# Kernel tuning notes

Hardware: AMD Instinct MI355X
Metric: run time of the kernel (lower is better)

Reference implementation:

```python
import jax, jax.numpy as jnp
import numpy as np

B, S, E, H = 4, 2048, 1024, 16
D = E // H  # head_dim = 64

def setup_inputs() -> dict:
    key = jax.random.key(0)
    k1, k2, k3 = jax.random.split(key, 3)
    x = jax.random.normal(k1, (B, S, E), dtype=jnp.float32)
    # nn.Linear(E, 3E, bias=False): y = x @ W^T; we store W already transposed as [E, 3E]
    w_qkv = jax.random.normal(k2, (E, 3 * E), dtype=jnp.float32) * (E ** -0.5)
    w_out = jax.random.normal(k3, (E, E), dtype=jnp.float32) * (E ** -0.5)
    b_out = jnp.zeros((E,), dtype=jnp.float32)
    return {"x": x, "w_qkv": w_qkv, "w_out": w_out, "b_out": b_out}

def reference(x, w_qkv, w_out, b_out):
    b, s, e = x.shape
    h, d = H, e // H
    # qkv projection then rearrange 'b s (qkv h d) -> qkv b h s d'
    qkv = (x @ w_qkv).reshape(b, s, 3, h, d).transpose(2, 0, 3, 1, 4)
    q, k, v = qkv[0], qkv[1], qkv[2]            # each [b, h, s, d]
    scale = jnp.asarray(d, x.dtype) ** -0.5
    att = jnp.einsum('bhxd,bhyd->bhxy', q, k) * scale   # [b, h, s, s]
    att = jax.nn.softmax(att, axis=-1)
    o = jnp.einsum('bhxy,bhyd->bhxd', att, v)           # [b, h, s, d]
    o = o.transpose(0, 2, 1, 3).reshape(b, s, e)        # 'b h s d -> b s (h d)'
    return o @ w_out + b_out
```

## Files before the change

kernel.cpp:

```cpp
#include <hip/hip_runtime.h>
#include <cstdint>
#include <cstddef>


typedef __attribute__((ext_vector_type(8))) short short8;
typedef __attribute__((ext_vector_type(4))) float float4_;
typedef unsigned int u32;
typedef unsigned short u16;

__device__ __forceinline__ u16 f2b(float f) {
  u32 u = __float_as_uint(f);
  u += 0x7FFFu + ((u >> 16) & 1u);
  return (u16)(u >> 16);
}

__device__ __forceinline__ float fexp2(float x) {
#if __has_builtin(__builtin_amdgcn_exp2f)
  return __builtin_amdgcn_exp2f(x);
#else
  return exp2f(x);
#endif
}

__device__ __forceinline__ u32 pk_trunc(float lo, float hi) {
#if __has_builtin(__builtin_amdgcn_perm)
  return __builtin_amdgcn_perm(__float_as_uint(hi), __float_as_uint(lo), 0x07060302);
#else
  return (__float_as_uint(hi) & 0xFFFF0000u) | (__float_as_uint(lo) >> 16);
#endif
}

#if __has_builtin(__builtin_amdgcn_fdot2_f32_bf16)
typedef __bf16 bf16x2 __attribute__((ext_vector_type(2)));
__device__ __forceinline__ float accum_pk(u32 pk, float acc) {
  bf16x2 p = __builtin_bit_cast(bf16x2, pk);
  bf16x2 one = __builtin_bit_cast(bf16x2, (u32)0x3F803F80u);
  return __builtin_amdgcn_fdot2_f32_bf16(p, one, acc, false);
}
#else
__device__ __forceinline__ float accum_pk(u32 pk, float acc) {
  return acc + __uint_as_float(pk << 16) + __uint_as_float(pk & 0xFFFF0000u);
}
#endif

__device__ __forceinline__ void async_cp16(const void* g, void* l) {
  __builtin_amdgcn_global_load_lds(
      (const __attribute__((address_space(1))) u32*)g,
      (__attribute__((address_space(3))) u32*)l, 16, 0, 0);
}


__device__ __forceinline__ void transpose_block(const float* __restrict__ in,
                                                u16* __restrict__ out,
                                                int R, int C, int bx, int by,
                                                float t[32][33]) {
  int tx = threadIdx.x & 31, ty = threadIdx.x >> 5;
  int r0 = by * 32, c0 = bx * 32;
#pragma unroll
  for (int k = 0; k < 4; k++)
    t[ty + 8 * k][tx] = in[(size_t)(r0 + ty + 8 * k) * C + c0 + tx];
  __syncthreads();
#pragma unroll
  for (int k = 0; k < 4; k++)
    out[(size_t)(c0 + ty + 8 * k) * R + r0 + tx] = f2b(t[tx][ty + 8 * k]);
}

__global__ void prepass_kernel(const float* __restrict__ x, u16* __restrict__ Xb,
                               const float* __restrict__ wqkv, u16* __restrict__ Wqt,
                               const float* __restrict__ wout, u16* __restrict__ Wot) {
  __shared__ float t[32][33];
  int gid = blockIdx.x;
  if (gid < 8192) {
    int i = gid * 256 + threadIdx.x;
    float4 v = ((const float4*)x)[i];
    uint2 p;
    p.x = (u32)f2b(v.x) | ((u32)f2b(v.y) << 16);
    p.y = (u32)f2b(v.z) | ((u32)f2b(v.w) << 16);
    ((uint2*)Xb)[i] = p;
  } else if (gid < 11264) {
    int j = gid - 8192;
    transpose_block(wqkv, Wqt, 1024, 3072, j % 96, j / 96, t);
  } else {
    int j = gid - 11264;
    transpose_block(wout, Wot, 1024, 1024, j % 32, j / 32, t);
  }
}

__global__ void transpose_v(const u16* __restrict__ V, u16* __restrict__ Vt) {
  __shared__ u16 t[64][80];
  int bh = blockIdx.y, s0 = blockIdx.x * 64;
  const u16* Vh = V + (size_t)bh * 2048 * 64;
  u16* Vth = Vt + (size_t)bh * 64 * 2048;
  int tr = threadIdx.x >> 3;
  int tc = (threadIdx.x & 7) * 8;
#pragma unroll
  for (int p = 0; p < 2; p++) {
    int r = p * 32 + tr;
    *(uint4*)&t[r][tc] = *(const uint4*)(Vh + (size_t)(s0 + r) * 64 + tc);
  }
  __syncthreads();
#pragma unroll
  for (int p = 0; p < 2; p++) {
    int d = p * 32 + tr;
    u16 tmp[8];
#pragma unroll
    for (int k = 0; k < 8; k++) tmp[k] = t[tc + k][d];
    *(uint4*)(Vth + (size_t)d * 2048 + s0 + tc) = *(uint4*)tmp;
  }
}


__global__ __launch_bounds__(512, 2) void gemm_qkv_kernel(
    const u16* __restrict__ A, const u16* __restrict__ Bt,
    u16* __restrict__ QKV) {
  const int K = 1024;
  const int NT = 16;
  __shared__ short8 lA[2][1024];
  __shared__ short8 lB[3][2048];
  int tid = threadIdx.x;
  int wid = tid >> 6, l = tid & 63, lr = l & 15, lq = l >> 4;
  int wm = wid >> 2, wn = wid & 3;
  int gid = blockIdx.x;
  int xcd = gid & 7, j = gid >> 3;
  int nt = j % 12, mt = xcd * 8 + j / 12;
  int m0 = mt * 128, n0 = nt * 256;

  float4_ acc[4][4] = {};

  const u16* srcA[2];
  const u16* srcB[4];
#pragma unroll
  for (int s = 0; s < 2; s++) {
    int fl = s * 8 + wid;
    srcA[s] = A + (size_t)(m0 + (fl >> 1) * 16 + lr) * K + (fl & 1) * 32 + lq * 8;
  }
#pragma unroll
  for (int s = 0; s < 4; s++) {
    int fl = s * 8 + wid;
    srcB[s] = Bt + (size_t)(n0 + (fl >> 1) * 16 + lr) * K + (fl & 1) * 32 + lq * 8;
  }

  auto stageA = [&](int buf, int k0) {
#pragma unroll
    for (int s = 0; s < 2; s++)
      async_cp16(srcA[s] + k0, &lA[buf][(s * 8 + wid) * 64 + l]);
  };
  auto stageB = [&](int bb, int k0) {
#pragma unroll
    for (int s = 0; s < 4; s++)
      async_cp16(srcB[s] + k0, &lB[bb][(s * 8 + wid) * 64 + l]);
  };

  stageA(0, 0);
  stageB(0, 0);
  stageB(1, 64);
  asm volatile("s_waitcnt vmcnt(4)" ::: "memory");
  __builtin_amdgcn_s_barrier();

  for (int u = 0; u < NT; ++u) {
    int buf = u & 1;
    int vb = u % 3;
    int kA = (u + 1 < NT ? u + 1 : NT - 1) * 64;
    int kB = (u + 2 < NT ? u + 2 : NT - 1) * 64;
    short8 af[4], bf[4];

#pragma unroll
    for (int mf = 0; mf < 4; mf++) af[mf] = lA[buf][((wm * 4 + mf) * 2 + 0) * 64 + l];
#pragma unroll
    for (int nf = 0; nf < 4; nf++) bf[nf] = lB[vb][((wn * 4 + nf) * 2 + 0) * 64 + l];
    stageA(buf ^ 1, kA);
    __builtin_amdgcn_s_barrier();
    __builtin_amdgcn_s_setprio(1);
#pragma unroll
    for (int mf = 0; mf < 4; mf++)
#pragma unroll
      for (int nf = 0; nf < 4; nf++)
        acc[mf][nf] = __builtin_amdgcn_mfma_f32_16x16x32_bf16(af[mf], bf[nf], acc[mf][nf], 0, 0, 0);
    __builtin_amdgcn_s_setprio(0);
    __builtin_amdgcn_s_barrier();

#pragma unroll
    for (int mf = 0; mf < 4; mf++) af[mf] = lA[buf][((wm * 4 + mf) * 2 + 1) * 64 + l];
#pragma unroll
    for (int nf = 0; nf < 4; nf++) bf[nf] = lB[vb][((wn * 4 + nf) * 2 + 1) * 64 + l];
    stageB((u + 2) % 3, kB);
    __builtin_amdgcn_s_barrier();
    __builtin_amdgcn_s_setprio(1);
#pragma unroll
    for (int mf = 0; mf < 4; mf++)
#pragma unroll
      for (int nf = 0; nf < 4; nf++)
        acc[mf][nf] = __builtin_amdgcn_mfma_f32_16x16x32_bf16(af[mf], bf[nf], acc[mf][nf], 0, 0, 0);
    __builtin_amdgcn_s_setprio(0);
    asm volatile("s_waitcnt vmcnt(4)" ::: "memory");
    __builtin_amdgcn_s_barrier();
  }
  asm volatile("s_waitcnt vmcnt(0)" ::: "memory");

  const float qsc = 0.18033688011112042f;
#pragma unroll
  for (int nf = 0; nf < 4; nf++) {
    int gn = n0 + wn * 64 + nf * 16 + lr;
    int sel = gn >> 10;
    int h = (gn >> 6) & 15;
    int d = gn & 63;
    float sc = (sel == 0) ? qsc : 1.0f;
    u16* dst = QKV + (size_t)sel * 8388608 + ((size_t)h * 2048) * 64 + d;
#pragma unroll
    for (int mf = 0; mf < 4; mf++) {
#pragma unroll
      for (int r = 0; r < 4; r++) {
        int gm = m0 + wm * 64 + mf * 16 + lq * 4 + r;
        int b = gm >> 11, s = gm & 2047;
        dst[((size_t)b * 16 * 2048 + s) * 64] = f2b(acc[mf][nf][r] * sc);
      }
    }
  }
}


__global__ __launch_bounds__(512, 2) void gemm_out_kernel(
    const u16* __restrict__ A, const u16* __restrict__ Bt,
    const float* __restrict__ bias, float* __restrict__ out) {
  const int K = 1024;
  const int NT = 16;
  __shared__ short8 lA[2][1024];
  __shared__ short8 lB[3][2048];
  int tid = threadIdx.x;
  int wid = tid >> 6, l = tid & 63, lr = l & 15, lq = l >> 4;
  int wm = wid >> 2, wn = wid & 3;
  int gid = blockIdx.x;
  int xcd = gid & 7, j = gid >> 3;
  int nt = j % 4, mt = xcd * 8 + j / 4;
  int m0 = mt * 128, n0 = nt * 256;

  float4_ acc[4][4] = {};

  const u16* srcA[2];
  const u16* srcB[4];
#pragma unroll
  for (int s = 0; s < 2; s++) {
    int fl = s * 8 + wid;
    srcA[s] = A + (size_t)(m0 + (fl >> 1) * 16 + lr) * K + (fl & 1) * 32 + lq * 8;
  }
#pragma unroll
  for (int s = 0; s < 4; s++) {
    int fl = s * 8 + wid;
    srcB[s] = Bt + (size_t)(n0 + (fl >> 1) * 16 + lr) * K + (fl & 1) * 32 + lq * 8;
  }

  auto stageA = [&](int buf, int k0) {
#pragma unroll
    for (int s = 0; s < 2; s++)
      async_cp16(srcA[s] + k0, &lA[buf][(s * 8 + wid) * 64 + l]);
  };
  auto stageB = [&](int bb, int k0) {
#pragma unroll
    for (int s = 0; s < 4; s++)
      async_cp16(srcB[s] + k0, &lB[bb][(s * 8 + wid) * 64 + l]);
  };

  stageA(0, 0);
  stageB(0, 0);
  stageB(1, 64);
  asm volatile("s_waitcnt vmcnt(4)" ::: "memory");
  __builtin_amdgcn_s_barrier();

  for (int u = 0; u < NT; ++u) {
    int buf = u & 1;
    int vb = u % 3;
    int kA = (u + 1 < NT ? u + 1 : NT - 1) * 64;
    int kB = (u + 2 < NT ? u + 2 : NT - 1) * 64;
    short8 af[4], bf[4];

#pragma unroll
    for (int mf = 0; mf < 4; mf++) af[mf] = lA[buf][((wm * 4 + mf) * 2 + 0) * 64 + l];
#pragma unroll
    for (int nf = 0; nf < 4; nf++) bf[nf] = lB[vb][((wn * 4 + nf) * 2 + 0) * 64 + l];
    stageA(buf ^ 1, kA);
    __builtin_amdgcn_s_barrier();
    __builtin_amdgcn_s_setprio(1);
#pragma unroll
    for (int mf = 0; mf < 4; mf++)
#pragma unroll
      for (int nf = 0; nf < 4; nf++)
        acc[mf][nf] = __builtin_amdgcn_mfma_f32_16x16x32_bf16(af[mf], bf[nf], acc[mf][nf], 0, 0, 0);
    __builtin_amdgcn_s_setprio(0);
    __builtin_amdgcn_s_barrier();

#pragma unroll
    for (int mf = 0; mf < 4; mf++) af[mf] = lA[buf][((wm * 4 + mf) * 2 + 1) * 64 + l];
#pragma unroll
    for (int nf = 0; nf < 4; nf++) bf[nf] = lB[vb][((wn * 4 + nf) * 2 + 1) * 64 + l];
    stageB((u + 2) % 3, kB);
    __builtin_amdgcn_s_barrier();
    __builtin_amdgcn_s_setprio(1);
#pragma unroll
    for (int mf = 0; mf < 4; mf++)
#pragma unroll
      for (int nf = 0; nf < 4; nf++)
        acc[mf][nf] = __builtin_amdgcn_mfma_f32_16x16x32_bf16(af[mf], bf[nf], acc[mf][nf], 0, 0, 0);
    __builtin_amdgcn_s_setprio(0);
    asm volatile("s_waitcnt vmcnt(4)" ::: "memory");
    __builtin_amdgcn_s_barrier();
  }
  asm volatile("s_waitcnt vmcnt(0)" ::: "memory");

#pragma unroll
  for (int nf = 0; nf < 4; nf++) {
    int gn = n0 + wn * 64 + nf * 16 + lr;
    float bv = bias[gn];
#pragma unroll
    for (int mf = 0; mf < 4; mf++)
#pragma unroll
      for (int r = 0; r < 4; r++) {
        int gm = m0 + wm * 64 + mf * 16 + lq * 4 + r;
        out[(size_t)gm * 1024 + gn] = acc[mf][nf][r] + bv;
      }
  }
}


__global__ __launch_bounds__(256) void attn_kernel(
    const u16* __restrict__ Qb, const u16* __restrict__ Kb,
    const u16* __restrict__ Vt, u16* __restrict__ Ob) {
  const int S = 2048, D = 64;
  __shared__ short8 lK[2][512];
  __shared__ short8 lV[2][512];
  __shared__ __align__(16) u32 pb[4][16][20];
  int tid = threadIdx.x;
  int w = tid >> 6, l = tid & 63, lr = l & 15, lq = l >> 4;
  int gid = blockIdx.x;
  int xcd = gid & 7, j = gid >> 3;
  int bh = xcd * 8 + (j >> 4);
  int qblk = j & 15;
  int q0 = qblk * 128 + w * 32;
  const u16* Qh = Qb + (size_t)bh * S * D;
  const u16* Kh = Kb + (size_t)bh * S * D;
  const u16* Vh = Vt + (size_t)bh * D * S;

  short8 qf[2][2];
#pragma unroll
  for (int qg = 0; qg < 2; qg++) {
    qf[qg][0] = *(const short8*)(Qh + (q0 + qg * 16 + lr) * D + lq * 8);
    qf[qg][1] = *(const short8*)(Qh + (q0 + qg * 16 + lr) * D + 32 + lq * 8);
  }

  float ls[2][4] = {};
  float4_ o[2][4] = {};

  const u16* kg = Kh + (size_t)(((w >> 1) << 5) + 2 * lr + (w & 1)) * D + lq * 8;
  const u16* vg = Vh + (size_t)(w * 16 + lr) * S + lq * 8;

  auto stage = [&](int buf, int kv0) {
    async_cp16(kg + (size_t)kv0 * D, &lK[buf][(w * 2 + 0) * 64 + l]);
    async_cp16(kg + (size_t)kv0 * D + 32, &lK[buf][(w * 2 + 1) * 64 + l]);
    async_cp16(vg + kv0, &lV[buf][(w * 2 + 0) * 64 + l]);
    async_cp16(vg + kv0 + 32, &lV[buf][(w * 2 + 1) * 64 + l]);
  };

  auto compute = [&](int buf) {
#pragma unroll
    for (int sub = 0; sub < 2; sub++) {
      short8 ke0 = lK[buf][((sub * 2 + 0) * 2 + 0) * 64 + l];
      short8 ke1 = lK[buf][((sub * 2 + 0) * 2 + 1) * 64 + l];
      short8 ko0 = lK[buf][((sub * 2 + 1) * 2 + 0) * 64 + l];
      short8 ko1 = lK[buf][((sub * 2 + 1) * 2 + 1) * 64 + l];
#pragma unroll
      for (int qg = 0; qg < 2; qg++) {
        float4_ z = {0.f, 0.f, 0.f, 0.f};
        float4_ s0 = __builtin_amdgcn_mfma_f32_16x16x32_bf16(qf[qg][0], ke0, z, 0, 0, 0);
        s0 = __builtin_amdgcn_mfma_f32_16x16x32_bf16(qf[qg][1], ke1, s0, 0, 0, 0);
        float4_ s1 = __builtin_amdgcn_mfma_f32_16x16x32_bf16(qf[qg][0], ko0, z, 0, 0, 0);
        s1 = __builtin_amdgcn_mfma_f32_16x16x32_bf16(qf[qg][1], ko1, s1, 0, 0, 0);
#pragma unroll
        for (int r = 0; r < 4; r++) {
          float p0 = fexp2(s0[r]);
          float p1 = fexp2(s1[r]);
          u32 pk = pk_trunc(p0, p1);
          ls[qg][r] = accum_pk(pk, ls[qg][r]);
          pb[w][lq * 4 + r][lr] = pk;
        }
        short8 pa = *(const short8*)&pb[w][lr][lq * 4];
#pragma unroll
        for (int dt = 0; dt < 4; dt++)
          o[qg][dt] = __builtin_amdgcn_mfma_f32_16x16x32_bf16(
              pa, lV[buf][(dt * 2 + sub) * 64 + l], o[qg][dt], 0, 0, 0);
      }
    }
  };

  stage(0, 0);
  for (int kv0 = 0; kv0 < S; kv0 += 128) {
    __syncthreads();
    stage(1, kv0 + 64);
    compute(0);
    __syncthreads();
    if (kv0 + 128 < S) stage(0, kv0 + 128);
    compute(1);
  }

  int b = bh >> 4, h = bh & 15;
#pragma unroll
  for (int qg = 0; qg < 2; qg++) {
    float inv[4];
#pragma unroll
    for (int r = 0; r < 4; r++) {
      float s = ls[qg][r];
#pragma unroll
      for (int off = 1; off < 16; off <<= 1) s += __shfl_xor(s, off, 64);
      inv[r] = 1.0f / s;
    }
#pragma unroll
    for (int dt = 0; dt < 4; dt++)
#pragma unroll
      for (int r = 0; r < 4; r++) {
        int s_ = q0 + qg * 16 + lq * 4 + r;
        Ob[((size_t)(b * 2048 + s_)) * 1024 + h * 64 + dt * 16 + lr] =
            f2b(o[qg][dt][r] * inv[r]);
      }
  }
}


extern "C" void kernel_launch(void* const* d_in, const int* in_sizes, int n_in,
                              void* d_out, int out_size, void* d_ws, size_t ws_size,
                              hipStream_t stream) {
  const float* x     = (const float*)d_in[0];
  const float* w_qkv = (const float*)d_in[1];
  const float* w_out = (const float*)d_in[2];
  const float* b_out = (const float*)d_in[3];
  float* out = (float*)d_out;

  char* ws = (char*)d_ws;
  u16* Xb  = (u16*)(ws);
  u16* Wqt = (u16*)(ws + (16u << 20));
  u16* Wot = (u16*)(ws + (22u << 20));
  u16* QKV = (u16*)(ws + (24u << 20));
  u16* Qb  = QKV;
  u16* Kb  = QKV + 8388608;
  u16* Vb  = QKV + 16777216;
  u16* Vt  = (u16*)(ws + (72u << 20));
  u16* Ob  = Xb;

  prepass_kernel<<<12288, 256, 0, stream>>>(x, Xb, w_qkv, Wqt, w_out, Wot);
  gemm_qkv_kernel<<<768, 512, 0, stream>>>(Xb, Wqt, QKV);
  transpose_v<<<dim3(32, 64), 256, 0, stream>>>(Vb, Vt);
  attn_kernel<<<1024, 256, 0, stream>>>(Qb, Kb, Vt, Ob);
  gemm_out_kernel<<<256, 512, 0, stream>>>(Ob, Wot, b_out, out);
}
```

Before: 342.5 us.

## Shrink GEMM tiles to 128x128 with 4 waves and simple double buffering

Both projection GEMMs move from 128x256 tiles with 8 waves and a staggered A-double/B-triple buffer to 128x128 tiles with 4 waves. Each tile uses a single double-buffered A+B stage with one wait and barrier per k-step, and the setprio hints are dropped. Grid sizes double and the block-to-tile mapping changes. The aim is more blocks for better CU fill, less LDS per block and simpler synchronisation, at the cost of lower per-block data reuse and a shallower prefetch overlap.

After: 339.9 us. About the same (-0.8%).

```diff
diff --git a/kernel.cpp b/kernel.cpp
--- a/kernel.cpp
+++ b/kernel.cpp
@@ -110,90 +110,65 @@
 }
 
 
-__global__ __launch_bounds__(512, 2) void gemm_qkv_kernel(
+__global__ __launch_bounds__(256, 2) void gemm_qkv_kernel(
     const u16* __restrict__ A, const u16* __restrict__ Bt,
     u16* __restrict__ QKV) {
   const int K = 1024;
   const int NT = 16;
   __shared__ short8 lA[2][1024];
-  __shared__ short8 lB[3][2048];
+  __shared__ short8 lB[2][1024];
   int tid = threadIdx.x;
   int wid = tid >> 6, l = tid & 63, lr = l & 15, lq = l >> 4;
-  int wm = wid >> 2, wn = wid & 3;
+  int wm = wid & 1, wn = wid >> 1;
   int gid = blockIdx.x;
   int xcd = gid & 7, j = gid >> 3;
-  int nt = j % 12, mt = xcd * 8 + j / 12;
-  int m0 = mt * 128, n0 = nt * 256;
+  int mt = xcd * 8 + (j & 7);
+  int nt = j >> 3;
+  int m0 = mt * 128, n0 = nt * 128;
 
   float4_ acc[4][4] = {};
 
-  const u16* srcA[2];
+  const u16* srcA[4];
   const u16* srcB[4];
 #pragma unroll
-  for (int s = 0; s < 2; s++) {
-    int fl = s * 8 + wid;
+  for (int s = 0; s < 4; s++) {
+    int fl = s * 4 + wid;
     srcA[s] = A + (size_t)(m0 + (fl >> 1) * 16 + lr) * K + (fl & 1) * 32 + lq * 8;
-  }
-#pragma unroll
-  for (int s = 0; s < 4; s++) {
-    int fl = s * 8 + wid;
     srcB[s] = Bt + (size_t)(n0 + (fl >> 1) * 16 + lr) * K + (fl & 1) * 32 + lq * 8;
   }
 
-  auto stageA = [&](int buf, int k0) {
-#pragma unroll
-    for (int s = 0; s < 2; s++)
-      async_cp16(srcA[s] + k0, &lA[buf][(s * 8 + wid) * 64 + l]);
+  auto stage = [&](int buf, int k0) {
+#pragma unroll
+    for (int s = 0; s < 4; s++)
+      async_cp16(srcA[s] + k0, &lA[buf][(s * 4 + wid) * 64 + l]);
+#pragma unroll
+    for (int s = 0; s < 4; s++)
+      async_cp16(srcB[s] + k0, &lB[buf][(s * 4 + wid) * 64 + l]);
   };
-  auto stageB = [&](int bb, int k0) {
-#pragma unroll
-    for (int s = 0; s < 4; s++)
-      async_cp16(srcB[s] + k0, &lB[bb][(s * 8 + wid) * 64 + l]);
-  };
-
-  stageA(0, 0);
-  stageB(0, 0);
-  stageB(1, 64);
-  asm volatile("s_waitcnt vmcnt(4)" ::: "memory");
-  __builtin_amdgcn_s_barrier();
+
+  stage(0, 0);
+  stage(1, 64);
 
   for (int u = 0; u < NT; ++u) {
     int buf = u & 1;
-    int vb = u % 3;
-    int kA = (u + 1 < NT ? u + 1 : NT - 1) * 64;
-    int kB = (u + 2 < NT ? u + 2 : NT - 1) * 64;
+    asm volatile("s_waitcnt vmcnt(8)" ::: "memory");
+    __builtin_amdgcn_s_barrier();
     short8 af[4], bf[4];
-
-#pragma unroll
-    for (int mf = 0; mf < 4; mf++) af[mf] = lA[buf][((wm * 4 + mf) * 2 + 0) * 64 + l];
-#pragma unroll
-    for (int nf = 0; nf < 4; nf++) bf[nf] = lB[vb][((wn * 4 + nf) * 2 + 0) * 64 + l];
-    stageA(buf ^ 1, kA);
+#pragma unroll
+    for (int ks = 0; ks < 2; ks++) {
+#pragma unroll
+      for (int mf = 0; mf < 4; mf++) af[mf] = lA[buf][((wm * 4 + mf) * 2 + ks) * 64 + l];
+#pragma unroll
+      for (int nf = 0; nf < 4; nf++) bf[nf] = lB[buf][((wn * 4 + nf) * 2 + ks) * 64 + l];
+#pragma unroll
+      for (int mf = 0; mf < 4; mf++)
+#pragma unroll
+        for (int nf = 0; nf < 4; nf++)
+          acc[mf][nf] = __builtin_amdgcn_mfma_f32_16x16x32_bf16(af[mf], bf[nf], acc[mf][nf], 0, 0, 0);
+    }
     __builtin_amdgcn_s_barrier();
-    __builtin_amdgcn_s_setprio(1);
-#pragma unroll
-    for (int mf = 0; mf < 4; mf++)
-#pragma unroll
-      for (int nf = 0; nf < 4; nf++)
-        acc[mf][nf] = __builtin_amdgcn_mfma_f32_16x16x32_bf16(af[mf], bf[nf], acc[mf][nf], 0, 0, 0);
-    __builtin_amdgcn_s_setprio(0);
-    __builtin_amdgcn_s_barrier();
-
-#pragma unroll
-    for (int mf = 0; mf < 4; mf++) af[mf] = lA[buf][((wm * 4 + mf) * 2 + 1) * 64 + l];
-#pragma unroll
-    for (int nf = 0; nf < 4; nf++) bf[nf] = lB[vb][((wn * 4 + nf) * 2 + 1) * 64 + l];
-    stageB((u + 2) % 3, kB);
-    __builtin_amdgcn_s_barrier();
-    __builtin_amdgcn_s_setprio(1);
-#pragma unroll
-    for (int mf = 0; mf < 4; mf++)
-#pragma unroll
-      for (int nf = 0; nf < 4; nf++)
-        acc[mf][nf] = __builtin_amdgcn_mfma_f32_16x16x32_bf16(af[mf], bf[nf], acc[mf][nf], 0, 0, 0);
-    __builtin_amdgcn_s_setprio(0);
-    asm volatile("s_waitcnt vmcnt(4)" ::: "memory");
-    __builtin_amdgcn_s_barrier();
+    int kn = (u + 2 < NT ? u + 2 : NT - 1) * 64;
+    stage(buf, kn);
   }
   asm volatile("s_waitcnt vmcnt(0)" ::: "memory");
 
@@ -218,91 +193,65 @@
   }
 }
 
-
-__global__ __launch_bounds__(512, 2) void gemm_out_kernel(
+__global__ __launch_bounds__(256, 2) void gemm_out_kernel(
     const u16* __restrict__ A, const u16* __restrict__ Bt,
     const float* __restrict__ bias, float* __restrict__ out) {
   const int K = 1024;
   const int NT = 16;
   __shared__ short8 lA[2][1024];
-  __shared__ short8 lB[3][2048];
+  __shared__ short8 lB[2][1024];
   int tid = threadIdx.x;
   int wid = tid >> 6, l = tid & 63, lr = l & 15, lq = l >> 4;
-  int wm = wid >> 2, wn = wid & 3;
+  int wm = wid & 1, wn = wid >> 1;
   int gid = blockIdx.x;
   int xcd = gid & 7, j = gid >> 3;
-  int nt = j % 4, mt = xcd * 8 + j / 4;
-  int m0 = mt * 128, n0 = nt * 256;
+  int mt = xcd * 8 + (j & 7);
+  int nt = j >> 3;
+  int m0 = mt * 128, n0 = nt * 128;
 
   float4_ acc[4][4] = {};
 
-  const u16* srcA[2];
+  const u16* srcA[4];
   const u16* srcB[4];
 #pragma unroll
-  for (int s = 0; s < 2; s++) {
-    int fl = s * 8 + wid;
+  for (int s = 0; s < 4; s++) {
+    int fl = s * 4 + wid;
     srcA[s] = A + (size_t)(m0 + (fl >> 1) * 16 + lr) * K + (fl & 1) * 32 + lq * 8;
-  }
-#pragma unroll
-  for (int s = 0; s < 4; s++) {
-    int fl = s * 8 + wid;
     srcB[s] = Bt + (size_t)(n0 + (fl >> 1) * 16 + lr) * K + (fl & 1) * 32 + lq * 8;
   }
 
-  auto stageA = [&](int buf, int k0) {
-#pragma unroll
-    for (int s = 0; s < 2; s++)
-      async_cp16(srcA[s] + k0, &lA[buf][(s * 8 + wid) * 64 + l]);
+  auto stage = [&](int buf, int k0) {
+#pragma unroll
+    for (int s = 0; s < 4; s++)
+      async_cp16(srcA[s] + k0, &lA[buf][(s * 4 + wid) * 64 + l]);
+#pragma unroll
+    for (int s = 0; s < 4; s++)
+      async_cp16(srcB[s] + k0, &lB[buf][(s * 4 + wid) * 64 + l]);
   };
-  auto stageB = [&](int bb, int k0) {
-#pragma unroll
-    for (int s = 0; s < 4; s++)
-      async_cp16(srcB[s] + k0, &lB[bb][(s * 8 + wid) * 64 + l]);
-  };
-
-  stageA(0, 0);
-  stageB(0, 0);
-  stageB(1, 64);
-  asm volatile("s_waitcnt vmcnt(4)" ::: "memory");
-  __builtin_amdgcn_s_barrier();
+
+  stage(0, 0);
+  stage(1, 64);
 
   for (int u = 0; u < NT; ++u) {
     int buf = u & 1;
-    int vb = u % 3;
-    int kA = (u + 1 < NT ? u + 1 : NT - 1) * 64;
-    int kB = (u + 2 < NT ? u + 2 : NT - 1) * 64;
+    asm volatile("s_waitcnt vmcnt(8)" ::: "memory");
+    __builtin_amdgcn_s_barrier();
     short8 af[4], bf[4];
-
-#pragma unroll
-    for (int mf = 0; mf < 4; mf++) af[mf] = lA[buf][((wm * 4 + mf) * 2 + 0) * 64 + l];
-#pragma unroll
-    for (int nf = 0; nf < 4; nf++) bf[nf] = lB[vb][((wn * 4 + nf) * 2 + 0) * 64 + l];
-    stageA(buf ^ 1, kA);
+#pragma unroll
+    for (int ks = 0; ks < 2; ks++) {
+#pragma unroll
+      for (int mf = 0; mf < 4; mf++) af[mf] = lA[buf][((wm * 4 + mf) * 2 + ks) * 64 + l];
+#pragma unroll
+      for (int nf = 0; nf < 4; nf++) bf[nf] = lB[buf][((wn * 4 + nf) * 2 + ks) * 64 + l];
+#pragma unroll
+      for (int mf = 0; mf < 4; mf++)
+#pragma unroll
+        for (int nf = 0; nf < 4; nf++)
+          acc[mf][nf] = __builtin_amdgcn_mfma_f32_16x16x32_bf16(af[mf], bf[nf], acc[mf][nf], 0, 0, 0);
+    }
     __builtin_amdgcn_s_barrier();
-    __builtin_amdgcn_s_setprio(1);
-#pragma unroll
-    for (int mf = 0; mf < 4; mf++)
-#pragma unroll
-      for (int nf = 0; nf < 4; nf++)
-        acc[mf][nf] = __builtin_amdgcn_mfma_f32_16x16x32_bf16(af[mf], bf[nf], acc[mf][nf], 0, 0, 0);
-    __builtin_amdgcn_s_setprio(0);
-    __builtin_amdgcn_s_barrier();
-
-#pragma unroll
-    for (int mf = 0; mf < 4; mf++) af[mf] = lA[buf][((wm * 4 + mf) * 2 + 1) * 64 + l];
-#pragma unroll
-    for (int nf = 0; nf < 4; nf++) bf[nf] = lB[vb][((wn * 4 + nf) * 2 + 1) * 64 + l];
-    stageB((u + 2) % 3, kB);
-    __builtin_amdgcn_s_barrier();
-    __builtin_amdgcn_s_setprio(1);
-#pragma unroll
-    for (int mf = 0; mf < 4; mf++)
-#pragma unroll
-      for (int nf = 0; nf < 4; nf++)
-        acc[mf][nf] = __builtin_amdgcn_mfma_f32_16x16x32_bf16(af[mf], bf[nf], acc[mf][nf], 0, 0, 0);
-    __builtin_amdgcn_s_setprio(0);
-    asm volatile("s_waitcnt vmcnt(4)" ::: "memory");
-    __builtin_amdgcn_s_barrier();
+    int kn = (u + 2 < NT ? u + 2 : NT - 1) * 64;
+    stage(buf, kn);
   }
   asm volatile("s_waitcnt vmcnt(0)" ::: "memory");
 
@@ -444,8 +393,8 @@
   u16* Ob  = Xb;
 
   prepass_kernel<<<12288, 256, 0, stream>>>(x, Xb, w_qkv, Wqt, w_out, Wot);
-  gemm_qkv_kernel<<<768, 512, 0, stream>>>(Xb, Wqt, QKV);
+  gemm_qkv_kernel<<<1536, 256, 0, stream>>>(Xb, Wqt, QKV);
   transpose_v<<<dim3(32, 64), 256, 0, stream>>>(Vb, Vt);
   attn_kernel<<<1024, 256, 0, stream>>>(Qb, Kb, Vt, Ob);
-  gemm_out_kernel<<<256, 512, 0, stream>>>(Ob, Wot, b_out, out);
-}
+  gemm_out_kernel<<<512, 256, 0, stream>>>(Ob, Wot, b_out, out);
+}
```
